# Performance work log

Hardware: AMD Instinct MI355X
Metric: run time of the kernel (lower is better)

## Reference

```python
import jax, jax.numpy as jnp
import numpy as np

K = 3          # kernel size
PAD = 1        # padding


def _conv2d(x, w, b):
    # plain 3x3 conv, stride 1, pad 1, NCHW / OIHW
    out = jax.lax.conv_general_dilated(
        x, w, window_strides=(1, 1), padding=((PAD, PAD), (PAD, PAD)),
        dimension_numbers=('NCHW', 'OIHW', 'NCHW'))
    return out + b[None, :, None, None]


def _deform_conv2d(x, offsets, w, b):
    # torchvision deform_conv2d semantics (stride=1, dilation=1, no mask)
    B, C, H, W = x.shape
    K2 = K * K
    off = offsets.reshape(B, K2, 2, H, W)
    dy, dx = off[:, :, 0], off[:, :, 1]              # [B,K2,H,W], (y,x) order
    ki, kj = jnp.meshgrid(jnp.arange(K), jnp.arange(K), indexing='ij')
    ki = ki.reshape(K2).astype(x.dtype)
    kj = kj.reshape(K2).astype(x.dtype)
    base_y = (jnp.arange(H, dtype=x.dtype)[None, :, None] - PAD + ki[:, None, None])  # [K2,H,1]
    base_x = (jnp.arange(W, dtype=x.dtype)[None, None, :] - PAD + kj[:, None, None])  # [K2,1,W]
    py = base_y[None] + dy                            # [B,K2,H,W] sampling rows
    px = base_x[None] + dx                            # [B,K2,H,W] sampling cols

    y0 = jnp.floor(py); x0 = jnp.floor(px)
    y1 = y0 + 1.0;      x1 = x0 + 1.0
    wy1 = py - y0; wy0 = 1.0 - wy1
    wx1 = px - x0; wx0 = 1.0 - wx1

    def corner(yc, xc, wgt):
        valid = ((yc >= 0) & (yc <= H - 1) & (xc >= 0) & (xc <= W - 1))
        iy = jnp.clip(yc, 0, H - 1).astype(jnp.int32)
        ix = jnp.clip(xc, 0, W - 1).astype(jnp.int32)
        # per-batch gather: x[b][:, iy[b], ix[b]] -> [C,K2,H,W]
        vals = jax.vmap(lambda xb, iyb, ixb: xb[:, iyb, ixb])(x, iy, ix)
        return vals * (wgt * valid.astype(x.dtype))[:, None]  # [B,C,K2,H,W]

    sampled = (corner(y0, x0, wy0 * wx0) + corner(y0, x1, wy0 * wx1)
               + corner(y1, x0, wy1 * wx0) + corner(y1, x1, wy1 * wx1))
    out = jnp.einsum('bckhw,ock->bohw', sampled, w.reshape(w.shape[0], C, K2))
    return out + b[None, :, None, None]


def setup_inputs() -> dict:
    key = jax.random.key(0)
    ks = jax.random.split(key, 6)
    B, C, O, H, W = 4, 256, 256, 64, 64
    x = jax.random.normal(ks[0], (B, C, H, W), dtype=jnp.float32)
    y = jax.random.normal(ks[1], (B, C, H, W), dtype=jnp.float32)
    # offset conv predicts 2*K*K offset channels; small init keeps offsets a few px
    offset_w = jax.random.normal(ks[2], (2 * K * K, C, K, K), dtype=jnp.float32) * 0.01
    offset_b = jax.random.normal(ks[3], (2 * K * K,), dtype=jnp.float32) * 0.01
    deform_w = jax.random.normal(ks[4], (O, C, K, K), dtype=jnp.float32) * (1.0 / np.sqrt(C * K * K))
    deform_b = jax.random.normal(ks[5], (O,), dtype=jnp.float32) * 0.01
    return {"x": x, "y": y, "offset_w": offset_w, "offset_b": offset_b,
            "deform_w": deform_w, "deform_b": deform_b}


def reference(x, y, offset_w, offset_b, deform_w, deform_b):
    offsets = _conv2d(y, offset_w, offset_b)          # [B, 2*K*K, H, W]
    return _deform_conv2d(x, offsets, deform_w, deform_b)
```

## Files before the change

kernel.cpp:

```cpp
#include <hip/hip_runtime.h>
#include <hip/hip_bf16.h>
#include <stdint.h>


typedef __bf16 bf16x8 __attribute__((ext_vector_type(8)));
typedef float  f32x4  __attribute__((ext_vector_type(4)));

__device__ __forceinline__ unsigned short f2bfu(float f) {
    union { float f; unsigned u; } v; v.f = f;
    return (unsigned short)((v.u + 0x8000u) >> 16);
}
__device__ __forceinline__ float lo16(unsigned u) {
    union { unsigned u; float f; } v; v.u = u << 16; return v.f;
}
__device__ __forceinline__ float hi16(unsigned u) {
    union { unsigned u; float f; } v; v.u = u & 0xFFFF0000u; return v.f;
}
__device__ __forceinline__ unsigned cvtpk_bf16(float lo, float hi) {
    unsigned r;
    asm("v_cvt_pk_bf16_f32 %0, %1, %2" : "=v"(r) : "v"(lo), "v"(hi));
    return r;
}
__device__ __forceinline__ unsigned blend2(unsigned u0, unsigned u1, unsigned u2, unsigned u3,
                                           float4 w) {
    float lo = w.x * lo16(u0) + w.y * lo16(u1) + w.z * lo16(u2) + w.w * lo16(u3);
    float hi = w.x * hi16(u0) + w.y * hi16(u1) + w.z * hi16(u2) + w.w * hi16(u3);
    return cvtpk_bf16(lo, hi);
}

__global__ __launch_bounds__(256) void prep_kernel(
    const float* __restrict__ x, const float* __restrict__ y,
    const float* __restrict__ ow, const float* __restrict__ dw,
    unsigned short* __restrict__ xT, unsigned short* __restrict__ yT,
    unsigned short* __restrict__ Wp2, unsigned short* __restrict__ Bo)
{
    __shared__ float tile[64 * 69];
    int blk = blockIdx.x;
    int t = threadIdx.x;
    if (blk < 2048) {
        const float* src = x; unsigned short* dst = xT;
        if (blk >= 1024) { src = y; dst = yT; blk -= 1024; }
        int cq = blk & 3;
        int bh = blk >> 2;
        int w4 = t & 15, cl0 = t >> 4;
        const float* s = src + ((size_t)(bh >> 6) * 256 + cq * 64) * 4096 + (size_t)(bh & 63) * 64;
#pragma unroll
        for (int p = 0; p < 4; ++p) {
            int cl = p * 16 + cl0;
            float4 v = *(const float4*)&s[(size_t)cl * 4096 + w4 * 4];
            tile[(w4 * 4 + 0) * 69 + cl] = v.x;
            tile[(w4 * 4 + 1) * 69 + cl] = v.y;
            tile[(w4 * 4 + 2) * 69 + cl] = v.z;
            tile[(w4 * 4 + 3) * 69 + cl] = v.w;
        }
        __syncthreads();
        unsigned short* d = dst + (size_t)bh * 16384 + cq * 64;
#pragma unroll
        for (int p = 0; p < 4; ++p) {
            int w = p * 16 + cl0;
            float4 v = *(const float4*)&tile[w * 69 + w4 * 4];
            ushort4 r = make_ushort4(f2bfu(v.x), f2bfu(v.y), f2bfu(v.z), f2bfu(v.w));
            *(ushort4*)&d[w * 256 + w4 * 4] = r;
        }
    } else if (blk < 2336) {
        int tid = (blk - 2048) * 256 + t;
        int q8 = tid >> 8;
        int o  = tid & 255;
        int k0 = q8 * 8;
        int tap = k0 >> 8, c0 = k0 & 255;
        const float* s = dw + o * 2304 + c0 * 9 + tap;
        ushort4 r0 = make_ushort4(f2bfu(s[0]), f2bfu(s[9]), f2bfu(s[18]), f2bfu(s[27]));
        ushort4 r1 = make_ushort4(f2bfu(s[36]), f2bfu(s[45]), f2bfu(s[54]), f2bfu(s[63]));
        *(ushort4*)&Wp2[tid * 8 + 0] = r0;
        *(ushort4*)&Wp2[tid * 8 + 4] = r1;
    } else {
        int idx = (blk - 2336) * 256 + t;
        int j = idx & 7;
        int n = (idx >> 3) & 31;
        int lq = (idx >> 8) & 3;
        int kg = idx >> 10;
        int k = kg * 32 + lq * 8 + j;
        int tap = k >> 8, c = k & 255;
        float v = (n < 18) ? ow[n * 2304 + c * 9 + tap] : 0.f;
        Bo[idx] = f2bfu(v);
    }
}


struct GatherRegs { uint4 ga[2][4]; float4 gw[2]; };

__device__ __forceinline__ void issue_tap(GatherRegs& G, int tap, int t,
                                          const unsigned short* __restrict__ xtb, int c0,
                                          const float4* __restrict__ pw_lds,
                                          const int4* __restrict__ pi_lds)
{
#pragma unroll
    for (int it = 0; it < 2; ++it) {
        int pos = (t >> 5) + it * 32;
        G.gw[it] = pw_lds[tap * 64 + pos];
        int4 p = pi_lds[tap * 64 + pos];
        G.ga[it][0] = *(const uint4*)&xtb[p.x + c0];
        G.ga[it][1] = *(const uint4*)&xtb[p.y + c0];
        G.ga[it][2] = *(const uint4*)&xtb[p.z + c0];
        G.ga[it][3] = *(const uint4*)&xtb[p.w + c0];
    }
}

__device__ __forceinline__ void commit_tap(const GatherRegs& G, unsigned short* buf,
                                           int t, int gr)
{
#pragma unroll
    for (int it = 0; it < 2; ++it) {
        int pos = (t >> 5) + it * 32;
        uint4 res;
        res.x = blend2(G.ga[it][0].x, G.ga[it][1].x, G.ga[it][2].x, G.ga[it][3].x, G.gw[it]);
        res.y = blend2(G.ga[it][0].y, G.ga[it][1].y, G.ga[it][2].y, G.ga[it][3].y, G.gw[it]);
        res.z = blend2(G.ga[it][0].z, G.ga[it][1].z, G.ga[it][2].z, G.ga[it][3].z, G.gw[it]);
        res.w = blend2(G.ga[it][0].w, G.ga[it][1].w, G.ga[it][2].w, G.ga[it][3].w, G.gw[it]);
        *(uint4*)&buf[pos * 256 + (gr ^ (pos & 7)) * 8] = res;
    }
}

__device__ __forceinline__ void mfma_tap(f32x4 (&acc)[4][2],
                                         const unsigned short* __restrict__ Ab,
                                         const unsigned short* __restrict__ Wp2,
                                         int tap, int kh, int lq, int ln, int ns)
{
    __builtin_amdgcn_s_setprio(1);
#pragma unroll
    for (int kc = 0; kc < 4; ++kc) {
        int gbase = kh * 16 + kc * 4 + lq;
        bf16x8 af[4];
#pragma unroll
        for (int ms = 0; ms < 4; ++ms) {
            int row = ms * 16 + ln;
            af[ms] = *(const bf16x8*)&Ab[row * 256 + (gbase ^ (row & 7)) * 8];
        }
        int kg = tap * 8 + kh * 4 + kc;
        bf16x8 bfr[2];
#pragma unroll
        for (int nt = 0; nt < 2; ++nt)
            bfr[nt] = *(const bf16x8*)&Wp2[((kg * 4 + lq) * 256 + ns * 32 + nt * 16 + ln) * 8];
#pragma unroll
        for (int ms = 0; ms < 4; ++ms)
#pragma unroll
            for (int nt = 0; nt < 2; ++nt)
                acc[ms][nt] = __builtin_amdgcn_mfma_f32_16x16x32_bf16(af[ms], bfr[nt], acc[ms][nt], 0, 0, 0);
    }
    __builtin_amdgcn_s_setprio(0);
}

__global__ __launch_bounds__(1024) void deform_kernel(
    const unsigned short* __restrict__ xT,
    const unsigned short* __restrict__ yT,
    const unsigned short* __restrict__ Wp2,
    const unsigned short* __restrict__ Bo,
    const float* __restrict__ ob,
    const float* __restrict__ db,
    float* __restrict__ out)
{
    __shared__ __align__(16) unsigned char smem[149504];
    unsigned short* Abase = (unsigned short*)smem;
    float*  red = (float*)smem;
    float*  epi = (float*)smem;
    float4* pw_lds = (float4*)(smem + 131072);
    int4*   pi_lds = (int4*)(smem + 131072 + 9216);

    int blk = blockIdx.x;
    int lb = (blk & 7) * 32 + (blk >> 3);
    int b = lb >> 6, h = lb & 63;
    int t = threadIdx.x;
    int wv = t >> 6, lane = t & 63;
    int ln = lane & 15, lq = lane >> 4;

    const unsigned short* xtb = xT + (size_t)b * (64 * 64 * 256);

    {
        int kq = wv >> 1, mh = wv & 1;
        f32x4 oacc[2][2];
#pragma unroll
        for (int m16 = 0; m16 < 2; ++m16)
#pragma unroll
            for (int nt = 0; nt < 2; ++nt)
                oacc[m16][nt] = (f32x4){0.f, 0.f, 0.f, 0.f};
        for (int u = kq * 9; u < kq * 9 + 9; ++u) {
            int tap = u >> 3, kc = u & 7;
            int ki = tap / 3, kj = tap - ki * 3;
            int hr = h + ki - 1;
            bf16x8 b0 = *(const bf16x8*)&Bo[(tap * 8 + kc) * 1024 + lq * 256 + ln * 8];
            bf16x8 b1 = *(const bf16x8*)&Bo[(tap * 8 + kc) * 1024 + lq * 256 + (16 + ln) * 8];
#pragma unroll
            for (int m16 = 0; m16 < 2; ++m16) {
                int wr = mh * 32 + m16 * 16 + ln + kj - 1;
                bf16x8 af = (bf16x8)(__bf16)0.0f;
                if (hr >= 0 && hr < 64 && wr >= 0 && wr < 64)
                    af = *(const bf16x8*)&yT[((size_t)(b * 64 + hr) * 64 + wr) * 256 + kc * 32 + lq * 8];
                oacc[m16][0] = __builtin_amdgcn_mfma_f32_16x16x32_bf16(af, b0, oacc[m16][0], 0, 0, 0);
                oacc[m16][1] = __builtin_amdgcn_mfma_f32_16x16x32_bf16(af, b1, oacc[m16][1], 0, 0, 0);
            }
        }
        float* rz = red + (size_t)(kq * 2 + mh) * 1056;
#pragma unroll
        for (int m16 = 0; m16 < 2; ++m16)
#pragma unroll
            for (int nt = 0; nt < 2; ++nt) {
                int o_l = nt * 16 + ln;
#pragma unroll
                for (int r = 0; r < 4; ++r)
                    rz[o_l * 33 + m16 * 16 + lq * 4 + r] = oacc[m16][nt][r];
            }
    }
    __syncthreads();
    if (t < 576) {
        int tap = t >> 6, pos = t & 63;
        int mh_p = pos >> 5, pl = pos & 31;
        float dy = ob[2 * tap], dx = ob[2 * tap + 1];
#pragma unroll
        for (int kq = 0; kq < 8; ++kq) {
            const float* rz = red + (size_t)(kq * 2 + mh_p) * 1056;
            dy += rz[(2 * tap) * 33 + pl];
            dx += rz[(2 * tap + 1) * 33 + pl];
        }
        int ki = tap / 3, kj = tap - ki * 3;
        float py = (float)(h - 1 + ki) + dy;
        float px = (float)(pos - 1 + kj) + dx;
        float y0 = floorf(py), x0 = floorf(px);
        float wy1 = py - y0, wx1 = px - x0;
        float wy0 = 1.f - wy1, wx0 = 1.f - wx1;
        float y1 = y0 + 1.f, x1 = x0 + 1.f;
        float vy0 = (y0 >= 0.f && y0 <= 63.f) ? 1.f : 0.f;
        float vy1 = (y1 >= 0.f && y1 <= 63.f) ? 1.f : 0.f;
        float vx0 = (x0 >= 0.f && x0 <= 63.f) ? 1.f : 0.f;
        float vx1 = (x1 >= 0.f && x1 <= 63.f) ? 1.f : 0.f;
        int iy0 = (int)fminf(fmaxf(y0, 0.f), 63.f);
        int iy1 = (int)fminf(fmaxf(y1, 0.f), 63.f);
        int ix0 = (int)fminf(fmaxf(x0, 0.f), 63.f);
        int ix1 = (int)fminf(fmaxf(x1, 0.f), 63.f);
        pw_lds[t] = make_float4(wy0 * wx0 * vy0 * vx0, wy0 * wx1 * vy0 * vx1,
                                wy1 * wx0 * vy1 * vx0, wy1 * wx1 * vy1 * vx1);
        pi_lds[t] = make_int4((iy0 * 64 + ix0) * 256, (iy0 * 64 + ix1) * 256,
                              (iy1 * 64 + ix0) * 256, (iy1 * 64 + ix1) * 256);
    }
    __syncthreads();

    int ns = wv & 7, kh = wv >> 3;

    f32x4 acc[4][2];
#pragma unroll
    for (int ms = 0; ms < 4; ++ms)
#pragma unroll
        for (int nt = 0; nt < 2; ++nt)
            acc[ms][nt] = (f32x4){0.f, 0.f, 0.f, 0.f};

    int gr = t & 31, c0 = gr * 8;
    GatherRegs G;

    issue_tap(G, 0, t, xtb, c0, pw_lds, pi_lds);
    commit_tap(G, Abase + 0 * 16384, t, gr);
    issue_tap(G, 1, t, xtb, c0, pw_lds, pi_lds);
    commit_tap(G, Abase + 1 * 16384, t, gr);
    __syncthreads();

    for (int i = 0; i < 4; ++i) {
        int tp0 = 2 * i, tp1 = 2 * i + 1;
        int s0 = tp0 + 2, s1 = tp1 + 2;
        issue_tap(G, s0, t, xtb, c0, pw_lds, pi_lds);
        __builtin_amdgcn_sched_barrier(0);
        mfma_tap(acc, Abase + (tp0 & 3) * 16384, Wp2, tp0, kh, lq, ln, ns);
        __builtin_amdgcn_sched_barrier(0);
        commit_tap(G, Abase + (s0 & 3) * 16384, t, gr);
        if (s1 < 9) {
            issue_tap(G, s1, t, xtb, c0, pw_lds, pi_lds);
            __builtin_amdgcn_sched_barrier(0);
        }
        mfma_tap(acc, Abase + (tp1 & 3) * 16384, Wp2, tp1, kh, lq, ln, ns);
        __builtin_amdgcn_sched_barrier(0);
        if (s1 < 9)
            commit_tap(G, Abase + (s1 & 3) * 16384, t, gr);
        __syncthreads();
    }
    mfma_tap(acc, Abase + 0 * 16384, Wp2, 8, kh, lq, ln, ns);
    __syncthreads();

    if (kh == 1) {
        float* e = epi + (size_t)ns * 2176;
#pragma unroll
        for (int ms = 0; ms < 4; ++ms)
#pragma unroll
            for (int nt = 0; nt < 2; ++nt) {
                int o_l = nt * 16 + ln;
                f32x4 a = acc[ms][nt];
                *(float4*)&e[o_l * 68 + ms * 16 + lq * 4] = make_float4(a[0], a[1], a[2], a[3]);
            }
    }
    __syncthreads();
    if (kh == 0) {
        const float* e = epi + (size_t)ns * 2176;
#pragma unroll
        for (int ms = 0; ms < 4; ++ms)
#pragma unroll
            for (int nt = 0; nt < 2; ++nt) {
                int o_l = nt * 16 + ln;
                int o = ns * 32 + o_l;
                float bias = db[o];
                float4 p = *(const float4*)&e[o_l * 68 + ms * 16 + lq * 4];
                f32x4 a = acc[ms][nt];
                float4 st = make_float4(a[0] + p.x + bias, a[1] + p.y + bias,
                                        a[2] + p.z + bias, a[3] + p.w + bias);
                *(float4*)&out[((size_t)(b * 256 + o)) * 4096 + h * 64 + ms * 16 + lq * 4] = st;
            }
    }
}

extern "C" void kernel_launch(void* const* d_in, const int* in_sizes, int n_in,
                              void* d_out, int out_size, void* d_ws, size_t ws_size,
                              hipStream_t stream) {
    const float* x  = (const float*)d_in[0];
    const float* y  = (const float*)d_in[1];
    const float* ow = (const float*)d_in[2];
    const float* ob = (const float*)d_in[3];
    const float* dw = (const float*)d_in[4];
    const float* db = (const float*)d_in[5];
    float* out = (float*)d_out;

    char* ws = (char*)d_ws;
    unsigned short* xT  = (unsigned short*)(ws);
    unsigned short* yT  = (unsigned short*)(ws + 8388608);
    unsigned short* Wp2 = (unsigned short*)(ws + 16777216);
    unsigned short* Bo  = (unsigned short*)(ws + 16777216 + 1179648);

    hipLaunchKernelGGL(prep_kernel, dim3(2624), dim3(256), 0, stream,
                       x, y, ow, dw, xT, yT, Wp2, Bo);
    hipLaunchKernelGGL(deform_kernel, dim3(256), dim3(1024), 0, stream,
                       xT, yT, Wp2, Bo, ob, db, out);
}
```

Measured before the change: 131.1 us.

## Use packed FP32 FMA for bilinear blend and stagger wave gather/MFMA phases

Result: slower. 210.9 us (+60.9%).

```diff
diff --git a/kernel.cpp b/kernel.cpp
--- a/kernel.cpp
+++ b/kernel.cpp
@@ -5,6 +5,7 @@
 
 typedef __bf16 bf16x8 __attribute__((ext_vector_type(8)));
 typedef float  f32x4  __attribute__((ext_vector_type(4)));
+typedef float  f32x2  __attribute__((ext_vector_type(2)));
 
 __device__ __forceinline__ unsigned short f2bfu(float f) {
     union { float f; unsigned u; } v; v.f = f;
@@ -21,11 +22,28 @@
     asm("v_cvt_pk_bf16_f32 %0, %1, %2" : "=v"(r) : "v"(lo), "v"(hi));
     return r;
 }
-__device__ __forceinline__ unsigned blend2(unsigned u0, unsigned u1, unsigned u2, unsigned u3,
-                                           float4 w) {
-    float lo = w.x * lo16(u0) + w.y * lo16(u1) + w.z * lo16(u2) + w.w * lo16(u3);
-    float hi = w.x * hi16(u0) + w.y * hi16(u1) + w.z * hi16(u2) + w.w * hi16(u3);
-    return cvtpk_bf16(lo, hi);
+__device__ __forceinline__ f32x2 pk_mul(f32x2 a, f32x2 b) {
+    f32x2 d;
+    asm("v_pk_mul_f32 %0, %1, %2" : "=v"(d) : "v"(a), "v"(b));
+    return d;
+}
+__device__ __forceinline__ f32x2 pk_fma(f32x2 a, f32x2 b, f32x2 c) {
+    f32x2 d;
+    asm("v_pk_fma_f32 %0, %1, %2, %3" : "=v"(d) : "v"(a), "v"(b), "v"(c));
+    return d;
+}
+__device__ __forceinline__ unsigned blend2pk(unsigned u0, unsigned u1, unsigned u2, unsigned u3,
+                                             const f32x2* wp) {
+    f32x2 x;
+    x.x = lo16(u0); x.y = hi16(u0);
+    f32x2 acc = pk_mul(x, wp[0]);
+    x.x = lo16(u1); x.y = hi16(u1);
+    acc = pk_fma(x, wp[1], acc);
+    x.x = lo16(u2); x.y = hi16(u2);
+    acc = pk_fma(x, wp[2], acc);
+    x.x = lo16(u3); x.y = hi16(u3);
+    acc = pk_fma(x, wp[3], acc);
+    return cvtpk_bf16(acc.x, acc.y);
 }
 
 __global__ __launch_bounds__(256) void prep_kernel(
@@ -112,11 +130,16 @@
 #pragma unroll
     for (int it = 0; it < 2; ++it) {
         int pos = (t >> 5) + it * 32;
+        f32x2 wp[4];
+        wp[0].x = G.gw[it].x; wp[0].y = G.gw[it].x;
+        wp[1].x = G.gw[it].y; wp[1].y = G.gw[it].y;
+        wp[2].x = G.gw[it].z; wp[2].y = G.gw[it].z;
+        wp[3].x = G.gw[it].w; wp[3].y = G.gw[it].w;
         uint4 res;
-        res.x = blend2(G.ga[it][0].x, G.ga[it][1].x, G.ga[it][2].x, G.ga[it][3].x, G.gw[it]);
-        res.y = blend2(G.ga[it][0].y, G.ga[it][1].y, G.ga[it][2].y, G.ga[it][3].y, G.gw[it]);
-        res.z = blend2(G.ga[it][0].z, G.ga[it][1].z, G.ga[it][2].z, G.ga[it][3].z, G.gw[it]);
-        res.w = blend2(G.ga[it][0].w, G.ga[it][1].w, G.ga[it][2].w, G.ga[it][3].w, G.gw[it]);
+        res.x = blend2pk(G.ga[it][0].x, G.ga[it][1].x, G.ga[it][2].x, G.ga[it][3].x, wp);
+        res.y = blend2pk(G.ga[it][0].y, G.ga[it][1].y, G.ga[it][2].y, G.ga[it][3].y, wp);
+        res.z = blend2pk(G.ga[it][0].z, G.ga[it][1].z, G.ga[it][2].z, G.ga[it][3].z, wp);
+        res.w = blend2pk(G.ga[it][0].w, G.ga[it][1].w, G.ga[it][2].w, G.ga[it][3].w, wp);
         *(uint4*)&buf[pos * 256 + (gr ^ (pos & 7)) * 8] = res;
     }
 }
@@ -244,6 +267,7 @@
     __syncthreads();
 
     int ns = wv & 7, kh = wv >> 3;
+    int stag = ((wv >> 2) ^ wv) & 1;
 
     f32x4 acc[4][2];
 #pragma unroll
@@ -264,19 +288,35 @@
     for (int i = 0; i < 4; ++i) {
         int tp0 = 2 * i, tp1 = 2 * i + 1;
         int s0 = tp0 + 2, s1 = tp1 + 2;
-        issue_tap(G, s0, t, xtb, c0, pw_lds, pi_lds);
-        __builtin_amdgcn_sched_barrier(0);
-        mfma_tap(acc, Abase + (tp0 & 3) * 16384, Wp2, tp0, kh, lq, ln, ns);
-        __builtin_amdgcn_sched_barrier(0);
-        commit_tap(G, Abase + (s0 & 3) * 16384, t, gr);
-        if (s1 < 9) {
-            issue_tap(G, s1, t, xtb, c0, pw_lds, pi_lds);
-            __builtin_amdgcn_sched_barrier(0);
-        }
-        mfma_tap(acc, Abase + (tp1 & 3) * 16384, Wp2, tp1, kh, lq, ln, ns);
-        __builtin_amdgcn_sched_barrier(0);
-        if (s1 < 9)
-            commit_tap(G, Abase + (s1 & 3) * 16384, t, gr);
+        if (stag == 0) {
+            issue_tap(G, s0, t, xtb, c0, pw_lds, pi_lds);
+            __builtin_amdgcn_sched_barrier(0);
+            mfma_tap(acc, Abase + (tp0 & 3) * 16384, Wp2, tp0, kh, lq, ln, ns);
+            __builtin_amdgcn_sched_barrier(0);
+            commit_tap(G, Abase + (s0 & 3) * 16384, t, gr);
+            if (s1 < 9) {
+                issue_tap(G, s1, t, xtb, c0, pw_lds, pi_lds);
+                __builtin_amdgcn_sched_barrier(0);
+            }
+            mfma_tap(acc, Abase + (tp1 & 3) * 16384, Wp2, tp1, kh, lq, ln, ns);
+            __builtin_amdgcn_sched_barrier(0);
+            if (s1 < 9)
+                commit_tap(G, Abase + (s1 & 3) * 16384, t, gr);
+        } else {
+            issue_tap(G, s0, t, xtb, c0, pw_lds, pi_lds);
+            __builtin_amdgcn_sched_barrier(0);
+            commit_tap(G, Abase + (s0 & 3) * 16384, t, gr);
+            __builtin_amdgcn_sched_barrier(0);
+            mfma_tap(acc, Abase + (tp0 & 3) * 16384, Wp2, tp0, kh, lq, ln, ns);
+            __builtin_amdgcn_sched_barrier(0);
+            if (s1 < 9) {
+                issue_tap(G, s1, t, xtb, c0, pw_lds, pi_lds);
+                __builtin_amdgcn_sched_barrier(0);
+                commit_tap(G, Abase + (s1 & 3) * 16384, t, gr);
+                __builtin_amdgcn_sched_barrier(0);
+            }
+            mfma_tap(acc, Abase + (tp1 & 3) * 16384, Wp2, tp1, kh, lq, ln, ns);
+        }
         __syncthreads();
     }
     mfma_tap(acc, Abase + 0 * 16384, Wp2, 8, kh, lq, ln, ns);
```

## Specialize warps into gather producers and MFMA consumers per tap

Applied to the files above, without the earlier changes.

Result: slower. 138.6 us (+5.7%).

```diff
diff --git a/kernel.cpp b/kernel.cpp
--- a/kernel.cpp
+++ b/kernel.cpp
@@ -87,67 +87,72 @@
 }
 
 
-struct GatherRegs { uint4 ga[2][4]; float4 gw[2]; };
-
-__device__ __forceinline__ void issue_tap(GatherRegs& G, int tap, int t,
-                                          const unsigned short* __restrict__ xtb, int c0,
+__device__ __forceinline__ void prod_half(int tap, int bp, int gr, int c0,
+                                          const unsigned short* __restrict__ xtb,
                                           const float4* __restrict__ pw_lds,
-                                          const int4* __restrict__ pi_lds)
-{
+                                          const int4* __restrict__ pi_lds,
+                                          unsigned short* __restrict__ buf)
+{
+    uint4 ga[2][4]; float4 gw[2];
 #pragma unroll
     for (int it = 0; it < 2; ++it) {
-        int pos = (t >> 5) + it * 32;
-        G.gw[it] = pw_lds[tap * 64 + pos];
+        int pos = bp + it * 16;
+        gw[it] = pw_lds[tap * 64 + pos];
         int4 p = pi_lds[tap * 64 + pos];
-        G.ga[it][0] = *(const uint4*)&xtb[p.x + c0];
-        G.ga[it][1] = *(const uint4*)&xtb[p.y + c0];
-        G.ga[it][2] = *(const uint4*)&xtb[p.z + c0];
-        G.ga[it][3] = *(const uint4*)&xtb[p.w + c0];
-    }
-}
-
-__device__ __forceinline__ void commit_tap(const GatherRegs& G, unsigned short* buf,
-                                           int t, int gr)
-{
+        ga[it][0] = *(const uint4*)&xtb[p.x + c0];
+        ga[it][1] = *(const uint4*)&xtb[p.y + c0];
+        ga[it][2] = *(const uint4*)&xtb[p.z + c0];
+        ga[it][3] = *(const uint4*)&xtb[p.w + c0];
+    }
 #pragma unroll
     for (int it = 0; it < 2; ++it) {
-        int pos = (t >> 5) + it * 32;
+        int pos = bp + it * 16;
         uint4 res;
-        res.x = blend2(G.ga[it][0].x, G.ga[it][1].x, G.ga[it][2].x, G.ga[it][3].x, G.gw[it]);
-        res.y = blend2(G.ga[it][0].y, G.ga[it][1].y, G.ga[it][2].y, G.ga[it][3].y, G.gw[it]);
-        res.z = blend2(G.ga[it][0].z, G.ga[it][1].z, G.ga[it][2].z, G.ga[it][3].z, G.gw[it]);
-        res.w = blend2(G.ga[it][0].w, G.ga[it][1].w, G.ga[it][2].w, G.ga[it][3].w, G.gw[it]);
+        res.x = blend2(ga[it][0].x, ga[it][1].x, ga[it][2].x, ga[it][3].x, gw[it]);
+        res.y = blend2(ga[it][0].y, ga[it][1].y, ga[it][2].y, ga[it][3].y, gw[it]);
+        res.z = blend2(ga[it][0].z, ga[it][1].z, ga[it][2].z, ga[it][3].z, gw[it]);
+        res.w = blend2(ga[it][0].w, ga[it][1].w, ga[it][2].w, ga[it][3].w, gw[it]);
         *(uint4*)&buf[pos * 256 + (gr ^ (pos & 7)) * 8] = res;
     }
 }
 
-__device__ __forceinline__ void mfma_tap(f32x4 (&acc)[4][2],
+__device__ __forceinline__ void prod_tap(int tap, int p0, int gr, int c0,
+                                         const unsigned short* __restrict__ xtb,
+                                         const float4* __restrict__ pw_lds,
+                                         const int4* __restrict__ pi_lds,
+                                         unsigned short* __restrict__ buf)
+{
+    prod_half(tap, p0,      gr, c0, xtb, pw_lds, pi_lds, buf);
+    prod_half(tap, p0 + 32, gr, c0, xtb, pw_lds, pi_lds, buf);
+}
+
+__device__ __forceinline__ void cons_tap(f32x4 (&acc)[4][2],
                                          const unsigned short* __restrict__ Ab,
                                          const unsigned short* __restrict__ Wp2,
-                                         int tap, int kh, int lq, int ln, int ns)
-{
-    __builtin_amdgcn_s_setprio(1);
-#pragma unroll
-    for (int kc = 0; kc < 4; ++kc) {
-        int gbase = kh * 16 + kc * 4 + lq;
+                                         int tap, int lq, int ln, int ns)
+{
+#pragma unroll
+    for (int kc = 0; kc < 8; ++kc) {
+        int gbase = kc * 4 + lq;
         bf16x8 af[4];
 #pragma unroll
         for (int ms = 0; ms < 4; ++ms) {
             int row = ms * 16 + ln;
             af[ms] = *(const bf16x8*)&Ab[row * 256 + (gbase ^ (row & 7)) * 8];
         }
-        int kg = tap * 8 + kh * 4 + kc;
+        int kg = tap * 8 + kc;
         bf16x8 bfr[2];
 #pragma unroll
         for (int nt = 0; nt < 2; ++nt)
             bfr[nt] = *(const bf16x8*)&Wp2[((kg * 4 + lq) * 256 + ns * 32 + nt * 16 + ln) * 8];
+        __builtin_amdgcn_s_setprio(1);
 #pragma unroll
         for (int ms = 0; ms < 4; ++ms)
 #pragma unroll
             for (int nt = 0; nt < 2; ++nt)
                 acc[ms][nt] = __builtin_amdgcn_mfma_f32_16x16x32_bf16(af[ms], bfr[nt], acc[ms][nt], 0, 0, 0);
-    }
-    __builtin_amdgcn_s_setprio(0);
+        __builtin_amdgcn_s_setprio(0);
+    }
 }
 
 __global__ __launch_bounds__(1024) void deform_kernel(
@@ -162,7 +167,6 @@
     __shared__ __align__(16) unsigned char smem[149504];
     unsigned short* Abase = (unsigned short*)smem;
     float*  red = (float*)smem;
-    float*  epi = (float*)smem;
     float4* pw_lds = (float4*)(smem + 131072);
     int4*   pi_lds = (int4*)(smem + 131072 + 9216);
 
@@ -243,7 +247,10 @@
     }
     __syncthreads();
 
-    int ns = wv & 7, kh = wv >> 3;
+    int ns = wv & 7;
+    bool isProd = (wv >= 8);
+    int gr = t & 31, c0 = gr * 8;
+    int p0 = (t >> 5) & 15;
 
     f32x4 acc[4][2];
 #pragma unroll
@@ -252,61 +259,33 @@
         for (int nt = 0; nt < 2; ++nt)
             acc[ms][nt] = (f32x4){0.f, 0.f, 0.f, 0.f};
 
-    int gr = t & 31, c0 = gr * 8;
-    GatherRegs G;
-
-    issue_tap(G, 0, t, xtb, c0, pw_lds, pi_lds);
-    commit_tap(G, Abase + 0 * 16384, t, gr);
-    issue_tap(G, 1, t, xtb, c0, pw_lds, pi_lds);
-    commit_tap(G, Abase + 1 * 16384, t, gr);
+    if (isProd) {
+        prod_tap(0, p0, gr, c0, xtb, pw_lds, pi_lds, Abase + 0 * 16384);
+        prod_tap(1, p0, gr, c0, xtb, pw_lds, pi_lds, Abase + 1 * 16384);
+    }
     __syncthreads();
 
-    for (int i = 0; i < 4; ++i) {
-        int tp0 = 2 * i, tp1 = 2 * i + 1;
-        int s0 = tp0 + 2, s1 = tp1 + 2;
-        issue_tap(G, s0, t, xtb, c0, pw_lds, pi_lds);
-        __builtin_amdgcn_sched_barrier(0);
-        mfma_tap(acc, Abase + (tp0 & 3) * 16384, Wp2, tp0, kh, lq, ln, ns);
-        __builtin_amdgcn_sched_barrier(0);
-        commit_tap(G, Abase + (s0 & 3) * 16384, t, gr);
-        if (s1 < 9) {
-            issue_tap(G, s1, t, xtb, c0, pw_lds, pi_lds);
-            __builtin_amdgcn_sched_barrier(0);
-        }
-        mfma_tap(acc, Abase + (tp1 & 3) * 16384, Wp2, tp1, kh, lq, ln, ns);
-        __builtin_amdgcn_sched_barrier(0);
-        if (s1 < 9)
-            commit_tap(G, Abase + (s1 & 3) * 16384, t, gr);
+    for (int tap = 0; tap < 9; ++tap) {
+        if (isProd) {
+            if (tap < 7)
+                prod_tap(tap + 2, p0, gr, c0, xtb, pw_lds, pi_lds,
+                         Abase + ((tap + 2) & 3) * 16384);
+        } else {
+            cons_tap(acc, Abase + (tap & 3) * 16384, Wp2, tap, lq, ln, ns);
+        }
         __syncthreads();
     }
-    mfma_tap(acc, Abase + 0 * 16384, Wp2, 8, kh, lq, ln, ns);
-    __syncthreads();
-
-    if (kh == 1) {
-        float* e = epi + (size_t)ns * 2176;
+
+    if (!isProd) {
 #pragma unroll
         for (int ms = 0; ms < 4; ++ms)
 #pragma unroll
             for (int nt = 0; nt < 2; ++nt) {
-                int o_l = nt * 16 + ln;
+                int o = ns * 32 + nt * 16 + ln;
+                float bias = db[o];
                 f32x4 a = acc[ms][nt];
-                *(float4*)&e[o_l * 68 + ms * 16 + lq * 4] = make_float4(a[0], a[1], a[2], a[3]);
-            }
-    }
-    __syncthreads();
-    if (kh == 0) {
-        const float* e = epi + (size_t)ns * 2176;
-#pragma unroll
-        for (int ms = 0; ms < 4; ++ms)
-#pragma unroll
-            for (int nt = 0; nt < 2; ++nt) {
-                int o_l = nt * 16 + ln;
-                int o = ns * 32 + o_l;
-                float bias = db[o];
-                float4 p = *(const float4*)&e[o_l * 68 + ms * 16 + lq * 4];
-                f32x4 a = acc[ms][nt];
-                float4 st = make_float4(a[0] + p.x + bias, a[1] + p.y + bias,
-                                        a[2] + p.z + bias, a[3] + p.w + bias);
+                float4 st = make_float4(a[0] + bias, a[1] + bias,
+                                        a[2] + bias, a[3] + bias);
                 *(float4*)&out[((size_t)(b * 256 + o)) * 4096 + h * 64 + ms * 16 + lq * 4] = st;
             }
     }
```
